# Performance work log

Hardware: AMD Instinct MI355X
Metric: run time of the kernel (lower is better)

The kernel has to match this reference:

```python
import jax, jax.numpy as jnp
from jax import lax
import numpy as np

H = 161  # input_size == hidden_size per the torch module


def _lstm(x, w_ih, w_hh, b_ih, b_hh, reverse):
    """Single-direction LSTM matching torch.nn.LSTM gate order (i, f, g, o).
    x: [B, T, I] -> returns hidden states [B, T, H]."""
    # Precompute the input contribution for all timesteps in one GEMM.
    pre = jnp.einsum('bti,gi->btg', x, w_ih) + b_ih + b_hh  # [B, T, 4H]
    B = x.shape[0]

    def step(carry, p):
        h, c = carry
        gates = p + h @ w_hh.T  # [B, 4H]
        i, f, g, o = jnp.split(gates, 4, axis=-1)
        c = jax.nn.sigmoid(f) * c + jax.nn.sigmoid(i) * jnp.tanh(g)
        h = jax.nn.sigmoid(o) * jnp.tanh(c)
        return (h, c), h

    init = (jnp.zeros((B, H), x.dtype), jnp.zeros((B, H), x.dtype))
    _, hs = lax.scan(step, init, jnp.swapaxes(pre, 0, 1), reverse=reverse)
    return jnp.swapaxes(hs, 0, 1)  # [B, T, H]


def _block(h, p, relu):
    # p = (wih_f, whh_f, bih_f, bhh_f, wih_b, whh_b, bih_b, bhh_b, W, b)
    f = _lstm(h, p[0], p[1], p[2], p[3], reverse=False)
    b = _lstm(h, p[4], p[5], p[6], p[7], reverse=True)
    out = jnp.concatenate([f, b], axis=-1) @ p[8].T + p[9]  # Linear(2H -> H)
    if relu:
        out = jax.nn.relu(out)
    return out + h  # residual


def _forward(x, p1, p2, p3):
    h = _block(x, p1, relu=True)
    h = _block(h, p2, relu=True)
    h = _block(h, p3, relu=False)  # block 3: no ReLU before residual in the torch code
    return h


def setup_inputs() -> dict:
    key = jax.random.key(0)
    ks = iter(jax.random.split(key, 64))
    s = 1.0 / np.sqrt(H)  # torch LSTM/Linear default uniform init scale

    def u(shape):
        return jax.random.uniform(next(ks), shape, jnp.float32, -s, s)

    inp = {"x": jax.random.normal(next(ks), (32, 1000, H), jnp.float32)}
    shapes = [("wih_f", (4 * H, H)), ("whh_f", (4 * H, H)), ("bih_f", (4 * H,)), ("bhh_f", (4 * H,)),
              ("wih_b", (4 * H, H)), ("whh_b", (4 * H, H)), ("bih_b", (4 * H,)), ("bhh_b", (4 * H,)),
              ("W", (H, 2 * H)), ("bl", (H,))]
    for i in (1, 2, 3):
        for nm, sh in shapes:
            inp[f"l{i}_{nm}"] = u(sh)
    return inp


def reference(x,
              l1_wih_f, l1_whh_f, l1_bih_f, l1_bhh_f, l1_wih_b, l1_whh_b, l1_bih_b, l1_bhh_b, l1_W, l1_bl,
              l2_wih_f, l2_whh_f, l2_bih_f, l2_bhh_f, l2_wih_b, l2_whh_b, l2_bih_b, l2_bhh_b, l2_W, l2_bl,
              l3_wih_f, l3_whh_f, l3_bih_f, l3_bhh_f, l3_wih_b, l3_whh_b, l3_bih_b, l3_bhh_b, l3_W, l3_bl):
    p1 = (l1_wih_f, l1_whh_f, l1_bih_f, l1_bhh_f, l1_wih_b, l1_whh_b, l1_bih_b, l1_bhh_b, l1_W, l1_bl)
    p2 = (l2_wih_f, l2_whh_f, l2_bih_f, l2_bhh_f, l2_wih_b, l2_whh_b, l2_bih_b, l2_bhh_b, l2_W, l2_bl)
    p3 = (l3_wih_f, l3_whh_f, l3_bih_f, l3_bhh_f, l3_wih_b, l3_whh_b, l3_bih_b, l3_bhh_b, l3_W, l3_bl)
    return _forward(x, p1, p2, p3)
```

## Files before the change

### kernel.cpp

```cpp
#include <hip/hip_runtime.h>
#include <hip/hip_fp16.h>

#define H 161
#define G4 644
#define BB 32
#define TT 1000
#define M_TOT (BB*TT)
#define KXP 192
#define KLP 352
#define NWIH 1344
#define NPAIR 84
#define NVEC (NPAIR/4)

typedef _Float16 h2_t  __attribute__((ext_vector_type(2)));
typedef _Float16 f16x8 __attribute__((ext_vector_type(8)));
typedef float    f32x4 __attribute__((ext_vector_type(4)));

__device__ __forceinline__ h2_t bc_h2(unsigned int u) {
    return __builtin_bit_cast(h2_t, u);
}

__device__ __forceinline__ float dot2f(h2_t a, h2_t b, float c) {
#if __has_builtin(__builtin_amdgcn_fdot2)
    return __builtin_amdgcn_fdot2(a, b, c, false);
#else
    return c + (float)a[0] * (float)b[0] + (float)a[1] * (float)b[1];
#endif
}

__device__ __forceinline__ float tanh_f(float x) {
    return 1.0f - 2.0f / (__expf(2.0f * x) + 1.0f);
}

__device__ __forceinline__ void bar_lds() {
    __builtin_amdgcn_sched_barrier(0);
    asm volatile("s_waitcnt lgkmcnt(0)" ::: "memory");
    __builtin_amdgcn_s_barrier();
    __builtin_amdgcn_sched_barrier(0);
}

__global__ __launch_bounds__(256) void cvt_x(
    const float* __restrict__ in,
    __half* __restrict__ out)
{
    const int total = M_TOT * KXP;
    for (int idx = blockIdx.x * 256 + threadIdx.x; idx < total;
         idx += gridDim.x * 256) {
        int m = idx / KXP, k = idx - m * KXP;
        float v = (k < H) ? in[(size_t)m * H + k] : (k == H ? 1.f : 0.f);
        out[idx] = __float2half(v);
    }
}

__global__ __launch_bounds__(256) void cvt_wih(
    const float* __restrict__ wf, const float* __restrict__ wb,
    const float* __restrict__ bif, const float* __restrict__ bhf,
    const float* __restrict__ bib, const float* __restrict__ bhb,
    __half* __restrict__ out)
{
    const int total = NWIH * KXP;
    for (int idx = blockIdx.x * 256 + threadIdx.x; idx < total;
         idx += gridDim.x * 256) {
        int n = idx / KXP, k = idx - n * KXP;
        float v = 0.f;
        if (n < G4) {
            v = (k < H) ? wf[(size_t)n * H + k]
                        : (k == H ? bif[n] + bhf[n] : 0.f);
        } else if (n < 2 * G4) {
            int g = n - G4;
            v = (k < H) ? wb[(size_t)g * H + k]
                        : (k == H ? bib[g] + bhb[g] : 0.f);
        }
        out[idx] = __float2half(v);
    }
}

__global__ __launch_bounds__(256) void cvt_W(
    const float* __restrict__ W,
    __half* __restrict__ out)
{
    const int total = 192 * KLP;
    for (int idx = blockIdx.x * 256 + threadIdx.x; idx < total;
         idx += gridDim.x * 256) {
        int n = idx / KLP, k = idx - n * KLP;
        float v = (n < H && k < 2 * H) ? W[(size_t)n * (2 * H) + k] : 0.f;
        out[idx] = __float2half(v);
    }
}

__global__ __launch_bounds__(256) void pre_mfma(
    const __half* __restrict__ A16,
    const __half* __restrict__ Wih16,
    __half* __restrict__ pre)
{
    const int m0 = blockIdx.x * 64, n0 = blockIdx.y * 64;
    const int tid = threadIdx.x;
    const int wv = tid >> 6, l = tid & 63;
    const int wm = wv & 1, wn = wv >> 1;
    const int cl = l & 15, kg = l >> 4;

    const __half* ap = A16   + (size_t)(m0 + wm * 32 + cl) * KXP + kg * 8;
    const __half* wp = Wih16 + (size_t)(n0 + wn * 32 + cl) * KXP + kg * 8;

    f32x4 acc[2][2] = {};
    #pragma unroll
    for (int kt = 0; kt < 6; ++kt) {
        f16x8 w0 = *(const f16x8*)(wp + kt * 32);
        f16x8 w1 = *(const f16x8*)(wp + 16 * KXP + kt * 32);
        f16x8 x0 = *(const f16x8*)(ap + kt * 32);
        f16x8 x1 = *(const f16x8*)(ap + 16 * KXP + kt * 32);
        acc[0][0] = __builtin_amdgcn_mfma_f32_16x16x32_f16(w0, x0, acc[0][0], 0, 0, 0);
        acc[0][1] = __builtin_amdgcn_mfma_f32_16x16x32_f16(w0, x1, acc[0][1], 0, 0, 0);
        acc[1][0] = __builtin_amdgcn_mfma_f32_16x16x32_f16(w1, x0, acc[1][0], 0, 0, 0);
        acc[1][1] = __builtin_amdgcn_mfma_f32_16x16x32_f16(w1, x1, acc[1][1], 0, 0, 0);
    }

    #pragma unroll
    for (int sn = 0; sn < 2; ++sn)
        #pragma unroll
        for (int sm = 0; sm < 2; ++sm) {
            int n = n0 + wn * 32 + sn * 16 + kg * 4;
            int m = m0 + wm * 32 + sm * 16 + cl;
            if (n < 2 * G4) {
                int d = (n >= G4) ? 1 : 0;
                int g = n - d * G4;
                __half2 lo, hi;
                lo.x = __float2half(acc[sn][sm][0]);
                lo.y = __float2half(acc[sn][sm][1]);
                hi.x = __float2half(acc[sn][sm][2]);
                hi.y = __float2half(acc[sn][sm][3]);
                __half* dst = pre + ((size_t)d * M_TOT + m) * G4 + g;
                *(__half2*)dst = lo;
                *(__half2*)(dst + 2) = hi;
            }
        }
}

__global__ __launch_bounds__(256) void lin_mfma(
    const __half* __restrict__ Hc,
    const __half* __restrict__ W16,
    const float* __restrict__ bl,
    const float* __restrict__ res,
    float* __restrict__ out,
    int relu)
{
    const int m0 = blockIdx.x * 64, n0 = blockIdx.y * 64;
    const int tid = threadIdx.x;
    const int wv = tid >> 6, l = tid & 63;
    const int wm = wv & 1, wn = wv >> 1;
    const int cl = l & 15, kg = l >> 4;

    const __half* ap = Hc  + (size_t)(m0 + wm * 32 + cl) * KLP + kg * 8;
    const __half* wp = W16 + (size_t)(n0 + wn * 32 + cl) * KLP + kg * 8;

    f32x4 acc[2][2] = {};
    #pragma unroll
    for (int kt = 0; kt < 11; ++kt) {
        f16x8 w0 = *(const f16x8*)(wp + kt * 32);
        f16x8 w1 = *(const f16x8*)(wp + 16 * KLP + kt * 32);
        f16x8 x0 = *(const f16x8*)(ap + kt * 32);
        f16x8 x1 = *(const f16x8*)(ap + 16 * KLP + kt * 32);
        acc[0][0] = __builtin_amdgcn_mfma_f32_16x16x32_f16(w0, x0, acc[0][0], 0, 0, 0);
        acc[0][1] = __builtin_amdgcn_mfma_f32_16x16x32_f16(w0, x1, acc[0][1], 0, 0, 0);
        acc[1][0] = __builtin_amdgcn_mfma_f32_16x16x32_f16(w1, x0, acc[1][0], 0, 0, 0);
        acc[1][1] = __builtin_amdgcn_mfma_f32_16x16x32_f16(w1, x1, acc[1][1], 0, 0, 0);
    }

    #pragma unroll
    for (int sn = 0; sn < 2; ++sn)
        #pragma unroll
        for (int sm = 0; sm < 2; ++sm) {
            int nb = n0 + wn * 32 + sn * 16 + kg * 4;
            int m  = m0 + wm * 32 + sm * 16 + cl;
            #pragma unroll
            for (int r = 0; r < 4; ++r) {
                int n = nb + r;
                if (n < H) {
                    float v = acc[sn][sm][r] + bl[n];
                    if (relu) v = fmaxf(v, 0.f);
                    v += res[(size_t)m * H + n];
                    out[(size_t)m * H + n] = v;
                }
            }
        }
}

__global__ __launch_bounds__(704, 3) void lstm_scan(
    const __half* __restrict__ pre,
    const float* __restrict__ whh_f,
    const float* __restrict__ whh_b,
    __half* __restrict__ hcat)
{
    const int b = blockIdx.x;
    const int d = blockIdx.y;
    const int tid = threadIdx.x;
    const float* whh = d ? whh_b : whh_f;

    __shared__ __align__(16) unsigned int h_sh[NPAIR];
    __shared__ float gate_sh[G4];

    const bool active = tid < G4;
    h2_t w[NPAIR];
    if (active) {
        const float* row = whh + (size_t)tid * H;
        #pragma unroll
        for (int i = 0; i < NPAIR; ++i) {
            float w0 = (2 * i < H) ? row[2 * i] : 0.f;
            float w1 = (2 * i + 1 < H) ? row[2 * i + 1] : 0.f;
            h2_t v; v[0] = (_Float16)w0; v[1] = (_Float16)w1;
            w[i] = v;
        }
    }
    if (tid < NPAIR) h_sh[tid] = 0u;
    float c = 0.f;
    const __half* pb = pre + ((size_t)d * M_TOT + (size_t)b * TT) * G4;
    const bool is_g_gate = (tid >= 2 * H) && (tid < 3 * H);

    int t0 = d ? (TT - 1) : 0;
    __half pc = __half(0.0f);
    if (active) pc = pb[(long long)t0 * G4 + tid];
    __syncthreads();

    for (int ttt = 0; ttt < TT; ++ttt) {
        int t = d ? (TT - 1 - ttt) : ttt;
        int tn = d ? (t - 1) : (t + 1);
        __half pn = __half(0.0f);
        if (active) pn = pb[(long long)tn * G4 + tid];

        if (active) {
            float a0 = 0.f, a1 = 0.f, a2 = 0.f, a3 = 0.f;
            const uint4* hv = (const uint4*)h_sh;
            #pragma unroll
            for (int i = 0; i < NVEC; ++i) {
                uint4 hh = hv[i];
                a0 = dot2f(w[4 * i + 0], bc_h2(hh.x), a0);
                a1 = dot2f(w[4 * i + 1], bc_h2(hh.y), a1);
                a2 = dot2f(w[4 * i + 2], bc_h2(hh.z), a2);
                a3 = dot2f(w[4 * i + 3], bc_h2(hh.w), a3);
            }
            float acc = __half2float(pc) + (a0 + a1) + (a2 + a3);
            float xs = is_g_gate ? (acc + acc) : acc;
            float s = 1.0f / (1.0f + __expf(-xs));
            gate_sh[tid] = is_g_gate ? (s + s - 1.0f) : s;
        }
        bar_lds();
        if (tid < H) {
            float ig = gate_sh[tid];
            float fg = gate_sh[tid + H];
            float gg = gate_sh[tid + 2 * H];
            float og = gate_sh[tid + 3 * H];
            c = fg * c + ig * gg;
            float h = og * tanh_f(c);
            __half h16 = __float2half(h);
            hcat[((size_t)b * TT + t) * KLP + (size_t)d * H + tid] = h16;
            ((__half*)h_sh)[tid] = h16;
        }
        bar_lds();
        pc = pn;
    }
}

extern "C" void kernel_launch(void* const* d_in, const int* in_sizes, int n_in,
                              void* d_out, int out_size, void* d_ws, size_t ws_size,
                              hipStream_t stream) {
    const float* x = (const float*)d_in[0];

    char* ws = (char*)d_ws;
    __half* pre    = (__half*)ws;
    __half* hcat16 = (__half*)(ws + (size_t)2 * M_TOT * G4 * 2);
    __half* A16    = (__half*)((char*)hcat16 + (size_t)M_TOT * KLP * 2);
    __half* wih16  = (__half*)((char*)A16 + (size_t)M_TOT * KXP * 2);
    __half* W16    = (__half*)((char*)wih16 + (size_t)NWIH * KXP * 2);
    float*  bufA   = (float*)((char*)W16 + (size_t)192 * KLP * 2);
    float*  bufB   = bufA + (size_t)M_TOT * H;

    hipMemsetAsync(hcat16, 0, (size_t)M_TOT * KLP * sizeof(__half), stream);

    const float* cur = x;
    float* outs[3] = {bufA, bufB, (float*)d_out};

    for (int l = 0; l < 3; ++l) {
        const float* const* p = (const float* const*)(d_in + 1 + 10 * l);
        cvt_x  <<<2048, 256, 0, stream>>>(cur, A16);
        cvt_wih<<<256, 256, 0, stream>>>(p[0], p[4], p[2], p[3], p[6], p[7], wih16);
        cvt_W  <<<64, 256, 0, stream>>>(p[8], W16);

        pre_mfma<<<dim3(M_TOT / 64, 21), 256, 0, stream>>>(A16, wih16, pre);
        lstm_scan<<<dim3(32, 2), 704, 0, stream>>>(pre, p[1], p[5], hcat16);
        lin_mfma<<<dim3(M_TOT / 64, 3), 256, 0, stream>>>(
            hcat16, W16, p[9], cur, outs[l], (l < 2) ? 1 : 0);
        cur = outs[l];
    }
}
```

Measured before the change: 3.598 ms.

## Compute two gate rows per thread in LSTM scan, keep weights in AGPRs

```diff
diff --git a/kernel.cpp b/kernel.cpp
--- a/kernel.cpp
+++ b/kernel.cpp
@@ -2,6 +2,7 @@
 #include <hip/hip_fp16.h>
 
 #define H 161
+#define H2 322
 #define G4 644
 #define BB 32
 #define TT 1000
@@ -28,6 +29,9 @@
 #endif
 }
 
+__device__ __forceinline__ float sigm_f(float x) {
+    return 1.0f / (1.0f + __expf(-x));
+}
 __device__ __forceinline__ float tanh_f(float x) {
     return 1.0f - 2.0f / (__expf(2.0f * x) + 1.0f);
 }
@@ -185,7 +189,7 @@
         }
 }
 
-__global__ __launch_bounds__(704, 3) void lstm_scan(
+__global__ __launch_bounds__(384, 2) void lstm_scan(
     const __half* __restrict__ pre,
     const float* __restrict__ whh_f,
     const float* __restrict__ whh_b,
@@ -197,67 +201,100 @@
     const float* whh = d ? whh_b : whh_f;
 
     __shared__ __align__(16) unsigned int h_sh[NPAIR];
-    __shared__ float gate_sh[G4];
-
-    const bool active = tid < G4;
-    h2_t w[NPAIR];
-    if (active) {
-        const float* row = whh + (size_t)tid * H;
+    __shared__ float2 gsh[H];
+
+    const bool active = tid < H2;
+    const int L = active ? tid : (H2 - 1);
+    const bool low = (L < H);
+
+    unsigned int wa0[NPAIR], wa1[NPAIR];
+    {
+        const float* r0 = whh + (size_t)L * H;
+        const float* r1 = whh + (size_t)(L + H2) * H;
         #pragma unroll
         for (int i = 0; i < NPAIR; ++i) {
-            float w0 = (2 * i < H) ? row[2 * i] : 0.f;
-            float w1 = (2 * i + 1 < H) ? row[2 * i + 1] : 0.f;
-            h2_t v; v[0] = (_Float16)w0; v[1] = (_Float16)w1;
-            w[i] = v;
+            int k = 2 * i;
+            float a0 = (k < H) ? r0[k] : 0.f;
+            float a1 = (k + 1 < H) ? r0[k + 1] : 0.f;
+            float b0 = (k < H) ? r1[k] : 0.f;
+            float b1 = (k + 1 < H) ? r1[k + 1] : 0.f;
+            h2_t v0; v0[0] = (_Float16)a0; v0[1] = (_Float16)a1;
+            h2_t v1; v1[0] = (_Float16)b0; v1[1] = (_Float16)b1;
+            unsigned int u0 = __builtin_bit_cast(unsigned int, v0);
+            unsigned int u1 = __builtin_bit_cast(unsigned int, v1);
+            asm volatile("v_accvgpr_write_b32 %0, %1" : "=a"(wa0[i]) : "v"(u0));
+            asm volatile("v_accvgpr_write_b32 %0, %1" : "=a"(wa1[i]) : "v"(u1));
         }
     }
     if (tid < NPAIR) h_sh[tid] = 0u;
+
     float c = 0.f;
     const __half* pb = pre + ((size_t)d * M_TOT + (size_t)b * TT) * G4;
-    const bool is_g_gate = (tid >= 2 * H) && (tid < 3 * H);
-
-    int t0 = d ? (TT - 1) : 0;
-    __half pc = __half(0.0f);
-    if (active) pc = pb[(long long)t0 * G4 + tid];
+
+    #define LDP2(tt_, OL, OH) {                                             \
+        int tc_ = ((tt_) < TT) ? (tt_) : (TT - 1);                          \
+        int t_  = d ? (TT - 1 - tc_) : tc_;                                 \
+        size_t o_ = (size_t)t_ * G4;                                        \
+        OL = pb[o_ + L];                                                    \
+        OH = pb[o_ + L + H2];                                               \
+    }
+
+    __half p0l, p0h, p1l, p1h;
+    LDP2(0, p0l, p0h)
+    LDP2(1, p1l, p1h)
     __syncthreads();
 
-    for (int ttt = 0; ttt < TT; ++ttt) {
-        int t = d ? (TT - 1 - ttt) : ttt;
-        int tn = d ? (t - 1) : (t + 1);
-        __half pn = __half(0.0f);
-        if (active) pn = pb[(long long)tn * G4 + tid];
-
-        if (active) {
-            float a0 = 0.f, a1 = 0.f, a2 = 0.f, a3 = 0.f;
-            const uint4* hv = (const uint4*)h_sh;
-            #pragma unroll
-            for (int i = 0; i < NVEC; ++i) {
-                uint4 hh = hv[i];
-                a0 = dot2f(w[4 * i + 0], bc_h2(hh.x), a0);
-                a1 = dot2f(w[4 * i + 1], bc_h2(hh.y), a1);
-                a2 = dot2f(w[4 * i + 2], bc_h2(hh.z), a2);
-                a3 = dot2f(w[4 * i + 3], bc_h2(hh.w), a3);
-            }
-            float acc = __half2float(pc) + (a0 + a1) + (a2 + a3);
-            float xs = is_g_gate ? (acc + acc) : acc;
-            float s = 1.0f / (1.0f + __expf(-xs));
-            gate_sh[tid] = is_g_gate ? (s + s - 1.0f) : s;
-        }
-        bar_lds();
-        if (tid < H) {
-            float ig = gate_sh[tid];
-            float fg = gate_sh[tid + H];
-            float gg = gate_sh[tid + 2 * H];
-            float og = gate_sh[tid + 3 * H];
-            c = fg * c + ig * gg;
-            float h = og * tanh_f(c);
-            __half h16 = __float2half(h);
-            hcat[((size_t)b * TT + t) * KLP + (size_t)d * H + tid] = h16;
-            ((__half*)h_sh)[tid] = h16;
-        }
-        bar_lds();
-        pc = pn;
-    }
+    #define STEP(TTT, PL, PH) {                                             \
+        int t = d ? (TT - 1 - (TTT)) : (TTT);                               \
+        float a0 = __half2float(PL), a0b = 0.f;                             \
+        float a1 = __half2float(PH), a1b = 0.f;                             \
+        LDP2((TTT) + 2, PL, PH)                 \
+        const uint4* h4 = (const uint4*)h_sh;                               \
+        _Pragma("unroll")                                                   \
+        for (int i = 0; i < NVEC; ++i) {                                    \
+            uint4 hh = h4[i];                                               \
+            unsigned int u0, u1;                                            \
+            asm volatile("v_accvgpr_read_b32 %0, %1" : "=v"(u0) : "a"(wa0[4*i+0])); \
+            asm volatile("v_accvgpr_read_b32 %0, %1" : "=v"(u1) : "a"(wa1[4*i+0])); \
+            a0  = dot2f(bc_h2(u0), bc_h2(hh.x), a0);                        \
+            a1  = dot2f(bc_h2(u1), bc_h2(hh.x), a1);                        \
+            asm volatile("v_accvgpr_read_b32 %0, %1" : "=v"(u0) : "a"(wa0[4*i+1])); \
+            asm volatile("v_accvgpr_read_b32 %0, %1" : "=v"(u1) : "a"(wa1[4*i+1])); \
+            a0b = dot2f(bc_h2(u0), bc_h2(hh.y), a0b);                       \
+            a1b = dot2f(bc_h2(u1), bc_h2(hh.y), a1b);                       \
+            asm volatile("v_accvgpr_read_b32 %0, %1" : "=v"(u0) : "a"(wa0[4*i+2])); \
+            asm volatile("v_accvgpr_read_b32 %0, %1" : "=v"(u1) : "a"(wa1[4*i+2])); \
+            a0  = dot2f(bc_h2(u0), bc_h2(hh.z), a0);                        \
+            a1  = dot2f(bc_h2(u1), bc_h2(hh.z), a1);                        \
+            asm volatile("v_accvgpr_read_b32 %0, %1" : "=v"(u0) : "a"(wa0[4*i+3])); \
+            asm volatile("v_accvgpr_read_b32 %0, %1" : "=v"(u1) : "a"(wa1[4*i+3])); \
+            a0b = dot2f(bc_h2(u0), bc_h2(hh.w), a0b);                       \
+            a1b = dot2f(bc_h2(u1), bc_h2(hh.w), a1b);                       \
+        }                                                                   \
+        a0 += a0b; a1 += a1b;                                               \
+        float act0 = sigm_f(a0);                   \
+        float xs = low ? (a1 + a1) : a1;                                    \
+        float ss = sigm_f(xs);                                              \
+        float act1 = low ? (ss + ss - 1.0f) : ss;     \
+        if (active && !low) gsh[L - H] = make_float2(act0, act1);           \
+        bar_lds();                                                          \
+        if (tid < H) {                                                      \
+            float2 fo = gsh[tid];                             \
+            c = fo.x * c + act0 * act1;                     \
+            float hval = fo.y * tanh_f(c);                                  \
+            __half h16 = __float2half(hval);                                \
+            hcat[((size_t)b * TT + t) * KLP + (size_t)d * H + tid] = h16;   \
+            ((__half*)h_sh)[tid] = h16;                                     \
+        }                                                                   \
+        bar_lds();                                                          \
+    }
+
+    for (int base = 0; base < TT; base += 2) {
+        STEP(base,     p0l, p0h)
+        STEP(base + 1, p1l, p1h)
+    }
+    #undef STEP
+    #undef LDP2
 }
 
 extern "C" void kernel_launch(void* const* d_in, const int* in_sizes, int n_in,
@@ -286,7 +323,7 @@
         cvt_W  <<<64, 256, 0, stream>>>(p[8], W16);
 
         pre_mfma<<<dim3(M_TOT / 64, 21), 256, 0, stream>>>(A16, wih16, pre);
-        lstm_scan<<<dim3(32, 2), 704, 0, stream>>>(pre, p[1], p[5], hcat16);
+        lstm_scan<<<dim3(32, 2), 384, 0, stream>>>(pre, p[1], p[5], hcat16);
         lin_mfma<<<dim3(M_TOT / 64, 3), 256, 0, stream>>>(
             hcat16, W16, p[9], cur, outs[l], (l < 2) ? 1 : 0);
         cur = outs[l];
```

Measured after the change: 6.481 ms. 1.8x slower.

## Batch weight conversions, fuse fp16 activation write into linear, reuse A tiles in pre GEMM

Applied to the files above, without the earlier changes.

```diff
diff --git a/kernel.cpp b/kernel.cpp
--- a/kernel.cpp
+++ b/kernel.cpp
@@ -52,12 +52,27 @@
     }
 }
 
-__global__ __launch_bounds__(256) void cvt_wih(
-    const float* __restrict__ wf, const float* __restrict__ wb,
-    const float* __restrict__ bif, const float* __restrict__ bhf,
-    const float* __restrict__ bib, const float* __restrict__ bhb,
+__global__ __launch_bounds__(256) void cvt_wih3(
+    const float* __restrict__ wf0, const float* __restrict__ wb0,
+    const float* __restrict__ bif0, const float* __restrict__ bhf0,
+    const float* __restrict__ bib0, const float* __restrict__ bhb0,
+    const float* __restrict__ wf1, const float* __restrict__ wb1,
+    const float* __restrict__ bif1, const float* __restrict__ bhf1,
+    const float* __restrict__ bib1, const float* __restrict__ bhb1,
+    const float* __restrict__ wf2, const float* __restrict__ wb2,
+    const float* __restrict__ bif2, const float* __restrict__ bhf2,
+    const float* __restrict__ bib2, const float* __restrict__ bhb2,
     __half* __restrict__ out)
 {
+    const int l = blockIdx.y;
+    const float* wf  = (l == 0) ? wf0  : (l == 1) ? wf1  : wf2;
+    const float* wb  = (l == 0) ? wb0  : (l == 1) ? wb1  : wb2;
+    const float* bif = (l == 0) ? bif0 : (l == 1) ? bif1 : bif2;
+    const float* bhf = (l == 0) ? bhf0 : (l == 1) ? bhf1 : bhf2;
+    const float* bib = (l == 0) ? bib0 : (l == 1) ? bib1 : bib2;
+    const float* bhb = (l == 0) ? bhb0 : (l == 1) ? bhb1 : bhb2;
+    __half* o = out + (size_t)l * NWIH * KXP;
+
     const int total = NWIH * KXP;
     for (int idx = blockIdx.x * 256 + threadIdx.x; idx < total;
          idx += gridDim.x * 256) {
@@ -71,20 +86,25 @@
             v = (k < H) ? wb[(size_t)g * H + k]
                         : (k == H ? bib[g] + bhb[g] : 0.f);
         }
-        out[idx] = __float2half(v);
-    }
-}
-
-__global__ __launch_bounds__(256) void cvt_W(
-    const float* __restrict__ W,
+        o[idx] = __float2half(v);
+    }
+}
+
+__global__ __launch_bounds__(256) void cvt_W3(
+    const float* __restrict__ W0, const float* __restrict__ W1,
+    const float* __restrict__ W2,
     __half* __restrict__ out)
 {
+    const int l = blockIdx.y;
+    const float* W = (l == 0) ? W0 : (l == 1) ? W1 : W2;
+    __half* o = out + (size_t)l * 192 * KLP;
+
     const int total = 192 * KLP;
     for (int idx = blockIdx.x * 256 + threadIdx.x; idx < total;
          idx += gridDim.x * 256) {
         int n = idx / KLP, k = idx - n * KLP;
         float v = (n < H && k < 2 * H) ? W[(size_t)n * (2 * H) + k] : 0.f;
-        out[idx] = __float2half(v);
+        o[idx] = __float2half(v);
     }
 }
 
@@ -93,47 +113,56 @@
     const __half* __restrict__ Wih16,
     __half* __restrict__ pre)
 {
-    const int m0 = blockIdx.x * 64, n0 = blockIdx.y * 64;
+    const int m0 = blockIdx.x * 64;
+    const int n0b = blockIdx.y * 192;
     const int tid = threadIdx.x;
     const int wv = tid >> 6, l = tid & 63;
     const int wm = wv & 1, wn = wv >> 1;
     const int cl = l & 15, kg = l >> 4;
 
-    const __half* ap = A16   + (size_t)(m0 + wm * 32 + cl) * KXP + kg * 8;
-    const __half* wp = Wih16 + (size_t)(n0 + wn * 32 + cl) * KXP + kg * 8;
-
-    f32x4 acc[2][2] = {};
+    const __half* ap = A16 + (size_t)(m0 + wm * 32 + cl) * KXP + kg * 8;
+    f16x8 xa0[6], xa1[6];
     #pragma unroll
     for (int kt = 0; kt < 6; ++kt) {
-        f16x8 w0 = *(const f16x8*)(wp + kt * 32);
-        f16x8 w1 = *(const f16x8*)(wp + 16 * KXP + kt * 32);
-        f16x8 x0 = *(const f16x8*)(ap + kt * 32);
-        f16x8 x1 = *(const f16x8*)(ap + 16 * KXP + kt * 32);
-        acc[0][0] = __builtin_amdgcn_mfma_f32_16x16x32_f16(w0, x0, acc[0][0], 0, 0, 0);
-        acc[0][1] = __builtin_amdgcn_mfma_f32_16x16x32_f16(w0, x1, acc[0][1], 0, 0, 0);
-        acc[1][0] = __builtin_amdgcn_mfma_f32_16x16x32_f16(w1, x0, acc[1][0], 0, 0, 0);
-        acc[1][1] = __builtin_amdgcn_mfma_f32_16x16x32_f16(w1, x1, acc[1][1], 0, 0, 0);
-    }
-
-    #pragma unroll
-    for (int sn = 0; sn < 2; ++sn)
+        xa0[kt] = *(const f16x8*)(ap + kt * 32);
+        xa1[kt] = *(const f16x8*)(ap + 16 * KXP + kt * 32);
+    }
+
+    for (int nb = 0; nb < 3; ++nb) {
+        const int n0 = n0b + nb * 64;
+        const __half* wp = Wih16 + (size_t)(n0 + wn * 32 + cl) * KXP + kg * 8;
+
+        f32x4 acc[2][2] = {};
         #pragma unroll
-        for (int sm = 0; sm < 2; ++sm) {
-            int n = n0 + wn * 32 + sn * 16 + kg * 4;
-            int m = m0 + wm * 32 + sm * 16 + cl;
-            if (n < 2 * G4) {
-                int d = (n >= G4) ? 1 : 0;
-                int g = n - d * G4;
-                __half2 lo, hi;
-                lo.x = __float2half(acc[sn][sm][0]);
-                lo.y = __float2half(acc[sn][sm][1]);
-                hi.x = __float2half(acc[sn][sm][2]);
-                hi.y = __float2half(acc[sn][sm][3]);
-                __half* dst = pre + ((size_t)d * M_TOT + m) * G4 + g;
-                *(__half2*)dst = lo;
-                *(__half2*)(dst + 2) = hi;
+        for (int kt = 0; kt < 6; ++kt) {
+            f16x8 w0 = *(const f16x8*)(wp + kt * 32);
+            f16x8 w1 = *(const f16x8*)(wp + 16 * KXP + kt * 32);
+            acc[0][0] = __builtin_amdgcn_mfma_f32_16x16x32_f16(w0, xa0[kt], acc[0][0], 0, 0, 0);
+            acc[0][1] = __builtin_amdgcn_mfma_f32_16x16x32_f16(w0, xa1[kt], acc[0][1], 0, 0, 0);
+            acc[1][0] = __builtin_amdgcn_mfma_f32_16x16x32_f16(w1, xa0[kt], acc[1][0], 0, 0, 0);
+            acc[1][1] = __builtin_amdgcn_mfma_f32_16x16x32_f16(w1, xa1[kt], acc[1][1], 0, 0, 0);
+        }
+
+        #pragma unroll
+        for (int sn = 0; sn < 2; ++sn)
+            #pragma unroll
+            for (int sm = 0; sm < 2; ++sm) {
+                int n = n0 + wn * 32 + sn * 16 + kg * 4;
+                int m = m0 + wm * 32 + sm * 16 + cl;
+                if (n < 2 * G4) {
+                    int d = (n >= G4) ? 1 : 0;
+                    int g = n - d * G4;
+                    __half2 lo, hi;
+                    lo.x = __float2half(acc[sn][sm][0]);
+                    lo.y = __float2half(acc[sn][sm][1]);
+                    hi.x = __float2half(acc[sn][sm][2]);
+                    hi.y = __float2half(acc[sn][sm][3]);
+                    __half* dst = pre + ((size_t)d * M_TOT + m) * G4 + g;
+                    *(__half2*)dst = lo;
+                    *(__half2*)(dst + 2) = hi;
+                }
             }
-        }
+    }
 }
 
 __global__ __launch_bounds__(256) void lin_mfma(
@@ -142,7 +171,8 @@
     const float* __restrict__ bl,
     const float* __restrict__ res,
     float* __restrict__ out,
-    int relu)
+    __half* __restrict__ A16out,
+    int relu, int wr_a16)
 {
     const int m0 = blockIdx.x * 64, n0 = blockIdx.y * 64;
     const int tid = threadIdx.x;
@@ -180,6 +210,8 @@
                     if (relu) v = fmaxf(v, 0.f);
                     v += res[(size_t)m * H + n];
                     out[(size_t)m * H + n] = v;
+                    if (wr_a16)
+                        A16out[(size_t)m * KXP + n] = __float2half(v);
                 }
             }
         }
@@ -269,26 +301,35 @@
     __half* pre    = (__half*)ws;
     __half* hcat16 = (__half*)(ws + (size_t)2 * M_TOT * G4 * 2);
     __half* A16    = (__half*)((char*)hcat16 + (size_t)M_TOT * KLP * 2);
-    __half* wih16  = (__half*)((char*)A16 + (size_t)M_TOT * KXP * 2);
-    __half* W16    = (__half*)((char*)wih16 + (size_t)NWIH * KXP * 2);
-    float*  bufA   = (float*)((char*)W16 + (size_t)192 * KLP * 2);
+    __half* wih3   = (__half*)((char*)A16 + (size_t)M_TOT * KXP * 2);
+    __half* W3     = (__half*)((char*)wih3 + (size_t)3 * NWIH * KXP * 2);
+    float*  bufA   = (float*)((char*)W3 + (size_t)3 * 192 * KLP * 2);
     float*  bufB   = bufA + (size_t)M_TOT * H;
 
+    const float* const* p0 = (const float* const*)(d_in + 1);
+    const float* const* p1 = (const float* const*)(d_in + 11);
+    const float* const* p2 = (const float* const*)(d_in + 21);
+
     hipMemsetAsync(hcat16, 0, (size_t)M_TOT * KLP * sizeof(__half), stream);
-
+    cvt_x<<<2048, 256, 0, stream>>>(x, A16);
+    cvt_wih3<<<dim3(256, 3), 256, 0, stream>>>(
+        p0[0], p0[4], p0[2], p0[3], p0[6], p0[7],
+        p1[0], p1[4], p1[2], p1[3], p1[6], p1[7],
+        p2[0], p2[4], p2[2], p2[3], p2[6], p2[7], wih3);
+    cvt_W3<<<dim3(64, 3), 256, 0, stream>>>(p0[8], p1[8], p2[8], W3);
+
+    const float* const* ps[3] = {p0, p1, p2};
     const float* cur = x;
     float* outs[3] = {bufA, bufB, (float*)d_out};
 
     for (int l = 0; l < 3; ++l) {
-        const float* const* p = (const float* const*)(d_in + 1 + 10 * l);
-        cvt_x  <<<2048, 256, 0, stream>>>(cur, A16);
-        cvt_wih<<<256, 256, 0, stream>>>(p[0], p[4], p[2], p[3], p[6], p[7], wih16);
-        cvt_W  <<<64, 256, 0, stream>>>(p[8], W16);
-
-        pre_mfma<<<dim3(M_TOT / 64, 21), 256, 0, stream>>>(A16, wih16, pre);
+        const float* const* p = ps[l];
+        pre_mfma<<<dim3(M_TOT / 64, 7), 256, 0, stream>>>(
+            A16, wih3 + (size_t)l * NWIH * KXP, pre);
         lstm_scan<<<dim3(32, 2), 704, 0, stream>>>(pre, p[1], p[5], hcat16);
         lin_mfma<<<dim3(M_TOT / 64, 3), 256, 0, stream>>>(
-            hcat16, W16, p[9], cur, outs[l], (l < 2) ? 1 : 0);
+            hcat16, W3 + (size_t)l * 192 * KLP, p[9], cur, outs[l], A16,
+            (l < 2) ? 1 : 0, (l < 2) ? 1 : 0);
         cur = outs[l];
     }
 }
```

Result: faster. 3.478 ms (-3.3%).
